# Optimization experiments

Hardware: AMD Instinct MI355X
Metric: run time of the kernel (lower is better)

## Reference

```python
import jax, jax.numpy as jnp
import numpy as np

N_NODES = 50000
N_EDGES = 400000
FEAT = 64      # irreps_in modeled as 64 scalar channels; head_dim == FEAT
HEADS = 4


def setup_inputs() -> dict:
    key = jax.random.key(0)
    k = jax.random.split(key, 7)
    x = jax.random.normal(k[0], (N_NODES, FEAT), dtype=jnp.float32)
    edge_index = jax.random.randint(k[1], (2, N_EDGES), 0, N_NODES, dtype=jnp.int32)
    s = 1.0 / np.sqrt(FEAT)
    Wq = jax.random.normal(k[2], (HEADS, FEAT, FEAT), dtype=jnp.float32) * s
    Wk = jax.random.normal(k[3], (HEADS, FEAT, FEAT), dtype=jnp.float32) * s
    Wv = jax.random.normal(k[4], (HEADS, FEAT, FEAT), dtype=jnp.float32) * s
    Wout = jax.random.normal(k[5], (FEAT, FEAT), dtype=jnp.float32) * s
    return {"x": x, "Wq": Wq, "Wk": Wk, "Wv": Wv, "Wout": Wout, "edge_index": edge_index}


def reference(x, Wq, Wk, Wv, Wout, edge_index):
    # Per-node attention over graph neighbors. The torch module pads neighbors
    # into degree buckets and runs SDPA per bucket; mathematically this is a
    # segment (per-receiver) softmax over incoming edges, which we compute
    # directly without padding or bucket loops.
    sender, receiver = edge_index[0], edge_index[1]
    n = x.shape[0]
    scale = x.shape[1] ** -0.5  # head_dim == FEAT in the original module

    Q = jnp.einsum('nf,hfd->hnd', x, Wq)  # (H, N, F)
    K = jnp.einsum('nf,hfd->hnd', x, Wk)
    V = jnp.einsum('nf,hfd->hnd', x, Wv)

    # Edge scores: q_receiver . k_sender per head -> (E, H)
    s = jnp.einsum('hef,hef->eh', Q[:, receiver], K[:, sender]) * scale

    # Numerically stable segment softmax over each receiver's neighborhood.
    m = jax.ops.segment_max(s, receiver, num_segments=n)          # (N, H)
    p = jnp.exp(s - m[receiver])                                   # (E, H)
    denom = jax.ops.segment_sum(p, receiver, num_segments=n)      # (N, H)
    alpha = p / denom[receiver]                                    # (E, H)

    # Weighted message aggregation: (H, E, F) scattered to (H, N, F).
    msg = alpha.T[:, :, None] * V[:, sender]
    agg = jax.vmap(lambda mh: jax.ops.segment_sum(mh, receiver, num_segments=n))(msg)

    out = jnp.nan_to_num(agg.mean(axis=0))  # deg-0 nodes contribute zeros
    return x + out @ Wout
```

## Files before the change

### kernel.cpp

```cpp
#include <hip/hip_runtime.h>

#define FEAT 64
#define HEADS 4
#define CAP 64
#define LROW 520
#define TSTR 80

typedef __attribute__((ext_vector_type(8))) short short8;
typedef __attribute__((ext_vector_type(8))) __bf16 bf16x8;
typedef __attribute__((ext_vector_type(4))) float floatx4;
typedef __attribute__((ext_vector_type(2))) float float2v;
typedef unsigned short ushortT;

static __device__ __forceinline__ unsigned short f2bf(float f) {
    union { float f; unsigned int u; } v; v.f = f;
    unsigned int u = v.u;
    u = u + 0x7fffu + ((u >> 16) & 1u);
    return (unsigned short)(u >> 16);
}
static __device__ __forceinline__ float bfl(unsigned int u) {
    union { unsigned int u; float f; } v; v.u = u << 16; return v.f;
}
static __device__ __forceinline__ float bfh(unsigned int u) {
    union { unsigned int u; float f; } v; v.u = u & 0xffff0000u; return v.f;
}

template <int CTRL>
static __device__ __forceinline__ float dppadd(float v) {
    int y = __builtin_amdgcn_update_dpp(0, __builtin_bit_cast(int, v),
                                        CTRL, 0xf, 0xf, true);
    return v + __builtin_bit_cast(float, y);
}

__global__ __launch_bounds__(256) void k_init(const float* __restrict__ Wq,
        const float* __restrict__ Wk, const float* __restrict__ Wv,
        const float* __restrict__ Wout, short8* __restrict__ Wpack,
        short8* __restrict__ WoutPack, int4* __restrict__ deg4, int nslots) {
    int t = blockIdx.x * 256 + threadIdx.x;
    if (t < nslots) deg4[t] = make_int4(0, 0, 0, 0);
    int o = t;
    if (o < 12 * 2 * 4 * 64) {
        int lane = o & 63, dt = (o >> 6) & 3, kb = (o >> 8) & 1, m = o >> 9;
        int mat = m >> 2, h = m & 3;
        const float* src = (mat == 0) ? Wq : (mat == 1) ? Wk : Wv;
        src += (size_t)h * 64 * 64;
        int d = dt * 16 + (lane & 15);
        int kbase = kb * 32 + (lane >> 4) * 8;
        short8 val;
#pragma unroll
        for (int j = 0; j < 8; j++)
            val[j] = (short)f2bf(src[(kbase + j) * 64 + d]);
        Wpack[o] = val;
    } else if (o < 6144 + 512) {
        int idx = o - 6144;
        int lane = idx & 63, kb = (idx >> 6) & 1, nt = idx >> 7;
        int d = nt * 16 + (lane & 15);
        int kbase = kb * 32 + (lane >> 4) * 8;
        short8 val;
#pragma unroll
        for (int j = 0; j < 8; j++)
            val[j] = (short)f2bf(Wout[(kbase + j) * 64 + d]);
        WoutPack[idx] = val;
    }
}

__global__ __launch_bounds__(256, 3) void k_qkv(const float* __restrict__ x,
        const short8* __restrict__ Wpack, const int* __restrict__ send,
        const int* __restrict__ recv, int* __restrict__ deg,
        int* __restrict__ srt, ushortT* __restrict__ Qb, ushortT* __restrict__ KVb,
        int E) {
    __shared__ ushortT lds[16 * LROW];
    int w = threadIdx.x >> 6, lane = threadIdx.x & 63;
    int quad = lane >> 4, lrow = lane & 15;
    int ntile = blockIdx.x * 16;

    int e = blockIdx.x * 256 + threadIdx.x;
    int r_edge = 0, s_edge = 0, pos = CAP;
    if (e < E) {
        r_edge = recv[e];
        s_edge = send[e];
        pos = atomicAdd(&deg[r_edge], 1);
    }

    const float* xrow = x + (size_t)(ntile + lrow) * 64 + quad * 8;
    float4 fa = *(const float4*)(xrow);
    float4 fb = *(const float4*)(xrow + 4);
    float4 fc = *(const float4*)(xrow + 32);
    float4 fd = *(const float4*)(xrow + 36);

    short8 B[3][2][4];
#pragma unroll
    for (int mat = 0; mat < 3; mat++)
#pragma unroll
        for (int kb = 0; kb < 2; kb++)
#pragma unroll
            for (int dt = 0; dt < 4; dt++)
                B[mat][kb][dt] =
                    Wpack[(((mat * 4 + w) * 2 + kb) * 4 + dt) * 64 + lane];

    short8 a0 = {(short)f2bf(fa.x), (short)f2bf(fa.y), (short)f2bf(fa.z), (short)f2bf(fa.w),
                 (short)f2bf(fb.x), (short)f2bf(fb.y), (short)f2bf(fb.z), (short)f2bf(fb.w)};
    short8 a1 = {(short)f2bf(fc.x), (short)f2bf(fc.y), (short)f2bf(fc.z), (short)f2bf(fc.w),
                 (short)f2bf(fd.x), (short)f2bf(fd.y), (short)f2bf(fd.z), (short)f2bf(fd.w)};
    bf16x8 X0 = __builtin_bit_cast(bf16x8, a0);
    bf16x8 X1 = __builtin_bit_cast(bf16x8, a1);
#pragma unroll
    for (int mat = 0; mat < 3; mat++) {
#pragma unroll
        for (int dt = 0; dt < 4; dt++) {
            floatx4 acc = {0.f, 0.f, 0.f, 0.f};
            acc = __builtin_amdgcn_mfma_f32_16x16x32_bf16(
                __builtin_bit_cast(bf16x8, B[mat][0][dt]), X0, acc, 0, 0, 0);
            acc = __builtin_amdgcn_mfma_f32_16x16x32_bf16(
                __builtin_bit_cast(bf16x8, B[mat][1][dt]), X1, acc, 0, 0, 0);
            if (mat == 0) {
                unsigned int u01 = (unsigned)f2bf(acc[0] * 0.125f)
                                 | ((unsigned)f2bf(acc[1] * 0.125f) << 16);
                unsigned int u23 = (unsigned)f2bf(acc[2] * 0.125f)
                                 | ((unsigned)f2bf(acc[3] * 0.125f) << 16);
                *(uint2*)&lds[lrow * LROW + w * 64 + dt * 16 + quad * 4]
                    = make_uint2(u01, u23);
            } else {
                int p = __builtin_amdgcn_cvt_pk_fp8_f32(acc[0], acc[1], 0, false);
                p = __builtin_amdgcn_cvt_pk_fp8_f32(acc[2], acc[3], p, true);
                int slot = w * 16 + dt * 4 + quad;
                *(unsigned int*)&lds[lrow * LROW + 256 + slot * 4 + ((mat == 2) ? 2 : 0)]
                    = (unsigned int)p;
            }
        }
    }
    __syncthreads();
    {
        int u = threadIdx.x;
#pragma unroll
        for (int rep = 0; rep < 2; rep++, u += 256) {
            int row = u >> 5, idx = u & 31;
            uint4 val = *(const uint4*)&lds[row * LROW + idx * 8];
            *(uint4*)(Qb + ((size_t)(ntile + row)) * 256 + idx * 8) = val;
        }
    }
    {
        uint4* KVq = (uint4*)KVb;
        int u = threadIdx.x;
#pragma unroll
        for (int rep = 0; rep < 2; rep++, u += 256) {
            int row = u >> 5, idx = u & 31;
            uint4 val = *(const uint4*)&lds[row * LROW + 256 + idx * 8];
            KVq[(size_t)(ntile + row) * 32 + idx] = val;
        }
    }
    if (e < E && pos < CAP) srt[(size_t)r_edge * CAP + pos] = s_edge;
}

__global__ __launch_bounds__(256, 3) void k_attn(const ushortT* __restrict__ Qb,
        const ushortT* __restrict__ KVb, const short8* __restrict__ WoutPack,
        const int* __restrict__ deg, const int* __restrict__ srt,
        const float* __restrict__ x, float* __restrict__ out, int N) {
    __shared__ ushortT tl[16 * TSTR];
    int w = threadIdx.x >> 6, lane = threadIdx.x & 63;
    int hs = lane >> 5, hl = lane & 31, jj = hl & 7;
    int rb = blockIdx.x * 16;
    const uint4* KV4 = (const uint4*)KVb;

    int d_[2]; uint4 qu_[2]; int4 sf_[2], s2_[2]; const int* slots_[2];
#pragma unroll
    for (int p = 0; p < 2; p++) {
        int r = rb + w * 4 + p * 2 + hs;
        d_[p] = min(deg[r], CAP);
        slots_[p] = srt + (size_t)r * CAP;
        qu_[p] = ((const uint4*)(Qb + (size_t)r * 256))[hl];
        sf_[p] = *(const int4*)(slots_[p]);
        s2_[p] = *(const int4*)(slots_[p] + 4);
    }

    uint4 kv_[2][8];
#pragma unroll
    for (int p = 0; p < 2; p++) {
        int d = d_[p];
        int s0 = (0 < d) ? sf_[p].x : 0;
        int s1 = (1 < d) ? sf_[p].y : 0;
        int s2v = (2 < d) ? sf_[p].z : 0;
        int s3 = (3 < d) ? sf_[p].w : 0;
        int s4v = (4 < d) ? s2_[p].x : 0;
        int s5 = (5 < d) ? s2_[p].y : 0;
        int s6 = (6 < d) ? s2_[p].z : 0;
        int s7 = (7 < d) ? s2_[p].w : 0;
        kv_[p][0] = KV4[(size_t)s0 * 32 + hl];
        kv_[p][1] = KV4[(size_t)s1 * 32 + hl];
        kv_[p][2] = KV4[(size_t)s2v * 32 + hl];
        kv_[p][3] = KV4[(size_t)s3 * 32 + hl];
        kv_[p][4] = KV4[(size_t)s4v * 32 + hl];
        kv_[p][5] = KV4[(size_t)s5 * 32 + hl];
        kv_[p][6] = KV4[(size_t)s6 * 32 + hl];
        kv_[p][7] = KV4[(size_t)s7 * 32 + hl];
    }

#pragma unroll
    for (int p = 0; p < 2; p++) {
        int d = d_[p];
        uint4 qu = qu_[p];
        float2v q01 = {bfl(qu.x), bfh(qu.x)};
        float2v q23 = {bfl(qu.y), bfh(qu.y)};
        float2v q45 = {bfl(qu.z), bfh(qu.z)};
        float2v q67 = {bfl(qu.w), bfh(qu.w)};
        float2v acc01 = {0.f, 0.f}, acc23 = {0.f, 0.f};
        float2v acc45 = {0.f, 0.f}, acc67 = {0.f, 0.f};
        float den = 0.f;

#define PROC(kv, pmask)                                                   \
    {                                                                     \
        float2v kA = __builtin_amdgcn_cvt_pk_f32_fp8(kv.x, false);        \
        float2v kB = __builtin_amdgcn_cvt_pk_f32_fp8(kv.x, true);         \
        float2v kC = __builtin_amdgcn_cvt_pk_f32_fp8(kv.z, false);        \
        float2v kD = __builtin_amdgcn_cvt_pk_f32_fp8(kv.z, true);         \
        float2v d2 = q01 * kA;                                            \
        d2 += q23 * kB;                                                   \
        d2 += q45 * kC;                                                   \
        d2 += q67 * kD;                                                   \
        float sp = d2.x + d2.y;                                           \
        sp = dppadd<0xB1>(sp);                                            \
        sp = dppadd<0x4E>(sp);                                            \
        sp = dppadd<0x141>(sp);                                           \
        float pv = __expf(sp);                                            \
        pv = (pmask) ? pv : 0.f;                                          \
        float2v vA = __builtin_amdgcn_cvt_pk_f32_fp8(kv.y, false);        \
        float2v vB = __builtin_amdgcn_cvt_pk_f32_fp8(kv.y, true);         \
        float2v vC = __builtin_amdgcn_cvt_pk_f32_fp8(kv.w, false);        \
        float2v vD = __builtin_amdgcn_cvt_pk_f32_fp8(kv.w, true);         \
        float2v pp = {pv, pv};                                            \
        den += pv;                                                        \
        acc01 += pp * vA; acc23 += pp * vB;                               \
        acc45 += pp * vC; acc67 += pp * vD;                               \
    }
        PROC(kv_[p][0], 0 < d) PROC(kv_[p][1], 1 < d)
        PROC(kv_[p][2], 2 < d) PROC(kv_[p][3], 3 < d)
        PROC(kv_[p][4], 4 < d) PROC(kv_[p][5], 5 < d)
        PROC(kv_[p][6], 6 < d) PROC(kv_[p][7], 7 < d)

        for (int i = 8; i < d; i += 4) {
            int4 s4 = *(const int4*)(slots_[p] + i);
            int t0 = s4.x;
            int t1 = (i + 1 < d) ? s4.y : 0;
            int t2 = (i + 2 < d) ? s4.z : 0;
            int t3 = (i + 3 < d) ? s4.w : 0;
            uint4 ka = KV4[(size_t)t0 * 32 + hl];
            uint4 kb = KV4[(size_t)t1 * 32 + hl];
            uint4 kc = KV4[(size_t)t2 * 32 + hl];
            uint4 kd = KV4[(size_t)t3 * 32 + hl];
            PROC(ka, true) PROC(kb, i + 1 < d) PROC(kc, i + 2 < d) PROC(kd, i + 3 < d)
        }
#undef PROC
        float a0 = acc01.x, a1 = acc01.y, a2 = acc23.x, a3 = acc23.y;
        float a4 = acc45.x, a5 = acc45.y, a6 = acc67.x, a7 = acc67.y;
        float inv = (den > 0.f) ? 0.25f / den : 0.f;
        a0 *= inv; a1 *= inv; a2 *= inv; a3 *= inv;
        a4 *= inv; a5 *= inv; a6 *= inv; a7 *= inv;
        a0 = dppadd<0x128>(a0); a1 = dppadd<0x128>(a1);
        a2 = dppadd<0x128>(a2); a3 = dppadd<0x128>(a3);
        a4 = dppadd<0x128>(a4); a5 = dppadd<0x128>(a5);
        a6 = dppadd<0x128>(a6); a7 = dppadd<0x128>(a7);
        a0 += __shfl_xor(a0, 16); a1 += __shfl_xor(a1, 16);
        a2 += __shfl_xor(a2, 16); a3 += __shfl_xor(a3, 16);
        a4 += __shfl_xor(a4, 16); a5 += __shfl_xor(a5, 16);
        a6 += __shfl_xor(a6, 16); a7 += __shfl_xor(a7, 16);
        if (hl < 8) {
            int ridx = w * 4 + p * 2 + hs;
            uint4 tv;
            tv.x = (unsigned)f2bf(a0) | ((unsigned)f2bf(a1) << 16);
            tv.y = (unsigned)f2bf(a2) | ((unsigned)f2bf(a3) << 16);
            tv.z = (unsigned)f2bf(a4) | ((unsigned)f2bf(a5) << 16);
            tv.w = (unsigned)f2bf(a6) | ((unsigned)f2bf(a7) << 16);
            *(uint4*)&tl[ridx * TSTR + jj * 8] = tv;
        }
    }
    __syncthreads();

    int q = lane >> 4, c = lane & 15;
    short8 ta0 = *(const short8*)&tl[c * TSTR + q * 8];
    short8 ta1 = *(const short8*)&tl[c * TSTR + 32 + q * 8];
    short8 tb0 = WoutPack[(w * 2 + 0) * 64 + lane];
    short8 tb1 = WoutPack[(w * 2 + 1) * 64 + lane];
    floatx4 acc = {0.f, 0.f, 0.f, 0.f};
    acc = __builtin_amdgcn_mfma_f32_16x16x32_bf16(
        __builtin_bit_cast(bf16x8, ta0), __builtin_bit_cast(bf16x8, tb0), acc, 0, 0, 0);
    acc = __builtin_amdgcn_mfma_f32_16x16x32_bf16(
        __builtin_bit_cast(bf16x8, ta1), __builtin_bit_cast(bf16x8, tb1), acc, 0, 0, 0);
#pragma unroll
    for (int reg = 0; reg < 4; reg++) {
        size_t idx = (size_t)(rb + q * 4 + reg) * 64 + w * 16 + c;
        out[idx] = x[idx] + acc[reg];
    }
}

extern "C" void kernel_launch(void* const* d_in, const int* in_sizes, int n_in,
                              void* d_out, int out_size, void* d_ws, size_t ws_size,
                              hipStream_t stream) {
    const float* x    = (const float*)d_in[0];
    const float* Wq   = (const float*)d_in[1];
    const float* Wk   = (const float*)d_in[2];
    const float* Wv   = (const float*)d_in[3];
    const float* Wout = (const float*)d_in[4];
    const int*   ei   = (const int*)d_in[5];
    int N = in_sizes[0] / FEAT;
    int E = in_sizes[5] / 2;
    const int* send = ei;
    const int* recv = ei + E;

    char* ws = (char*)d_ws;
    size_t o = 0;
    auto alloc = [&](size_t bytes) {
        void* p = ws + o;
        o = (o + bytes + 255) & ~(size_t)255;
        return p;
    };
    ushortT* Qb      = (ushortT*)alloc((size_t)N * 256 * 2);
    ushortT* KVb     = (ushortT*)alloc((size_t)N * 512);
    short8* Wpack    = (short8*)alloc(6144 * sizeof(short8));
    short8* WoutPack = (short8*)alloc(512 * sizeof(short8));
    int* deg         = (int*)alloc((size_t)((N + 3) & ~3) * 4);
    int* srt         = (int*)alloc((size_t)N * CAP * 4);

    int nslots = ((N + 3) & ~3) / 4;
    k_init<<<64, 256, 0, stream>>>(Wq, Wk, Wv, Wout, Wpack, WoutPack,
                                   (int4*)deg, nslots);
    k_qkv<<<N / 16, 256, 0, stream>>>(x, Wpack, send, recv, deg, srt, Qb, KVb, E);
    k_attn<<<N / 16, 256, 0, stream>>>(Qb, KVb, WoutPack, deg, srt, x,
                                       (float*)d_out, N);
}
```

Baseline: 142.3 us.

## Split edge scatter from projection kernel and decouple neighbor gathers from degree

The fused QKV-plus-edge-scatter kernel becomes two kernels: a dedicated edge scatter that builds per-receiver slot lists, and a pure projection kernel that loads weight fragments just before each MFMA instead of preloading all of them into registers. In the attention kernel, the first eight K/V gathers no longer wait on the degree load: slot indices are clamped to the valid node range instead of being masked by degree, so the gathers can issue as soon as the slot lists arrive. This relies on the later per-degree masking to discard the garbage slots. It also relaxes the attention kernel's occupancy hint and projection launch bounds, at the cost of an extra kernel launch and some wasted gather bandwidth on low-degree nodes.

```diff
diff --git a/kernel.cpp b/kernel.cpp
--- a/kernel.cpp
+++ b/kernel.cpp
@@ -64,40 +64,29 @@
     }
 }
 
-__global__ __launch_bounds__(256, 3) void k_qkv(const float* __restrict__ x,
-        const short8* __restrict__ Wpack, const int* __restrict__ send,
+__global__ __launch_bounds__(256) void k_scatter(const int* __restrict__ send,
         const int* __restrict__ recv, int* __restrict__ deg,
-        int* __restrict__ srt, ushortT* __restrict__ Qb, ushortT* __restrict__ KVb,
-        int E) {
+        int* __restrict__ srt, int E) {
+    int e = blockIdx.x * 256 + threadIdx.x;
+    if (e >= E) return;
+    int r = recv[e];
+    int s = send[e];
+    int pos = atomicAdd(&deg[r], 1);
+    if (pos < CAP) srt[(size_t)r * CAP + pos] = s;
+}
+
+__global__ __launch_bounds__(256) void k_proj(const float* __restrict__ x,
+        const short8* __restrict__ Wpack, ushortT* __restrict__ Qb,
+        ushortT* __restrict__ KVb) {
     __shared__ ushortT lds[16 * LROW];
     int w = threadIdx.x >> 6, lane = threadIdx.x & 63;
     int quad = lane >> 4, lrow = lane & 15;
     int ntile = blockIdx.x * 16;
-
-    int e = blockIdx.x * 256 + threadIdx.x;
-    int r_edge = 0, s_edge = 0, pos = CAP;
-    if (e < E) {
-        r_edge = recv[e];
-        s_edge = send[e];
-        pos = atomicAdd(&deg[r_edge], 1);
-    }
-
     const float* xrow = x + (size_t)(ntile + lrow) * 64 + quad * 8;
     float4 fa = *(const float4*)(xrow);
     float4 fb = *(const float4*)(xrow + 4);
     float4 fc = *(const float4*)(xrow + 32);
     float4 fd = *(const float4*)(xrow + 36);
-
-    short8 B[3][2][4];
-#pragma unroll
-    for (int mat = 0; mat < 3; mat++)
-#pragma unroll
-        for (int kb = 0; kb < 2; kb++)
-#pragma unroll
-            for (int dt = 0; dt < 4; dt++)
-                B[mat][kb][dt] =
-                    Wpack[(((mat * 4 + w) * 2 + kb) * 4 + dt) * 64 + lane];
-
     short8 a0 = {(short)f2bf(fa.x), (short)f2bf(fa.y), (short)f2bf(fa.z), (short)f2bf(fa.w),
                  (short)f2bf(fb.x), (short)f2bf(fb.y), (short)f2bf(fb.z), (short)f2bf(fb.w)};
     short8 a1 = {(short)f2bf(fc.x), (short)f2bf(fc.y), (short)f2bf(fc.z), (short)f2bf(fc.w),
@@ -106,13 +95,16 @@
     bf16x8 X1 = __builtin_bit_cast(bf16x8, a1);
 #pragma unroll
     for (int mat = 0; mat < 3; mat++) {
+        int m = mat * 4 + w;
 #pragma unroll
         for (int dt = 0; dt < 4; dt++) {
             floatx4 acc = {0.f, 0.f, 0.f, 0.f};
+            short8 b0 = Wpack[((m * 2 + 0) * 4 + dt) * 64 + lane];
+            short8 b1 = Wpack[((m * 2 + 1) * 4 + dt) * 64 + lane];
             acc = __builtin_amdgcn_mfma_f32_16x16x32_bf16(
-                __builtin_bit_cast(bf16x8, B[mat][0][dt]), X0, acc, 0, 0, 0);
+                __builtin_bit_cast(bf16x8, b0), X0, acc, 0, 0, 0);
             acc = __builtin_amdgcn_mfma_f32_16x16x32_bf16(
-                __builtin_bit_cast(bf16x8, B[mat][1][dt]), X1, acc, 0, 0, 0);
+                __builtin_bit_cast(bf16x8, b1), X1, acc, 0, 0, 0);
             if (mat == 0) {
                 unsigned int u01 = (unsigned)f2bf(acc[0] * 0.125f)
                                  | ((unsigned)f2bf(acc[1] * 0.125f) << 16);
@@ -149,10 +141,9 @@
             KVq[(size_t)(ntile + row) * 32 + idx] = val;
         }
     }
-    if (e < E && pos < CAP) srt[(size_t)r_edge * CAP + pos] = s_edge;
-}
-
-__global__ __launch_bounds__(256, 3) void k_attn(const ushortT* __restrict__ Qb,
+}
+
+__global__ __launch_bounds__(256, 2) void k_attn(const ushortT* __restrict__ Qb,
         const ushortT* __restrict__ KVb, const short8* __restrict__ WoutPack,
         const int* __restrict__ deg, const int* __restrict__ srt,
         const float* __restrict__ x, float* __restrict__ out, int N) {
@@ -166,25 +157,24 @@
 #pragma unroll
     for (int p = 0; p < 2; p++) {
         int r = rb + w * 4 + p * 2 + hs;
-        d_[p] = min(deg[r], CAP);
         slots_[p] = srt + (size_t)r * CAP;
-        qu_[p] = ((const uint4*)(Qb + (size_t)r * 256))[hl];
         sf_[p] = *(const int4*)(slots_[p]);
         s2_[p] = *(const int4*)(slots_[p] + 4);
+        qu_[p] = ((const uint4*)(Qb + (size_t)r * 256))[hl];
+        d_[p] = min(deg[r], CAP);
     }
 
     uint4 kv_[2][8];
 #pragma unroll
     for (int p = 0; p < 2; p++) {
-        int d = d_[p];
-        int s0 = (0 < d) ? sf_[p].x : 0;
-        int s1 = (1 < d) ? sf_[p].y : 0;
-        int s2v = (2 < d) ? sf_[p].z : 0;
-        int s3 = (3 < d) ? sf_[p].w : 0;
-        int s4v = (4 < d) ? s2_[p].x : 0;
-        int s5 = (5 < d) ? s2_[p].y : 0;
-        int s6 = (6 < d) ? s2_[p].z : 0;
-        int s7 = (7 < d) ? s2_[p].w : 0;
+        int s0 = min(max(sf_[p].x, 0), N - 1);
+        int s1 = min(max(sf_[p].y, 0), N - 1);
+        int s2v = min(max(sf_[p].z, 0), N - 1);
+        int s3 = min(max(sf_[p].w, 0), N - 1);
+        int s4v = min(max(s2_[p].x, 0), N - 1);
+        int s5 = min(max(s2_[p].y, 0), N - 1);
+        int s6 = min(max(s2_[p].z, 0), N - 1);
+        int s7 = min(max(s2_[p].w, 0), N - 1);
         kv_[p][0] = KV4[(size_t)s0 * 32 + hl];
         kv_[p][1] = KV4[(size_t)s1 * 32 + hl];
         kv_[p][2] = KV4[(size_t)s2v * 32 + hl];
@@ -323,7 +313,8 @@
     int nslots = ((N + 3) & ~3) / 4;
     k_init<<<64, 256, 0, stream>>>(Wq, Wk, Wv, Wout, Wpack, WoutPack,
                                    (int4*)deg, nslots);
-    k_qkv<<<N / 16, 256, 0, stream>>>(x, Wpack, send, recv, deg, srt, Qb, KVb, E);
+    k_scatter<<<(E + 255) / 256, 256, 0, stream>>>(send, recv, deg, srt, E);
+    k_proj<<<N / 16, 256, 0, stream>>>(x, Wpack, Qb, KVb);
     k_attn<<<N / 16, 256, 0, stream>>>(Qb, KVb, WoutPack, deg, srt, x,
                                        (float*)d_out, N);
 }
```

Result: slower. 152.0 us (+6.8%).

## Compute Q projection inside attention kernel instead of materializing it globally

Applied to the files above, without the earlier changes.

The Q projection moves from the projection kernel into the attention kernel. Each block computes Q for its own 16 receiver rows with MFMA into shared memory, so the bf16 Q buffer is no longer written to and read back from global memory. Q is computed while the KV gathers are in flight, which may hide some of that latency, but it adds a __syncthreads and extra MFMA work to the attention kernel. The launch bounds also drop the min-blocks hint of 3 and weights are loaded per tile instead of held up front, which changes register pressure and occupancy.

```diff
diff --git a/kernel.cpp b/kernel.cpp
--- a/kernel.cpp
+++ b/kernel.cpp
@@ -3,7 +3,8 @@
 #define FEAT 64
 #define HEADS 4
 #define CAP 64
-#define LROW 520
+#define KROW 264
+#define QROW 264
 #define TSTR 80
 
 typedef __attribute__((ext_vector_type(8))) short short8;
@@ -64,12 +65,11 @@
     }
 }
 
-__global__ __launch_bounds__(256, 3) void k_qkv(const float* __restrict__ x,
+__global__ __launch_bounds__(256) void k_proj(const float* __restrict__ x,
         const short8* __restrict__ Wpack, const int* __restrict__ send,
         const int* __restrict__ recv, int* __restrict__ deg,
-        int* __restrict__ srt, ushortT* __restrict__ Qb, ushortT* __restrict__ KVb,
-        int E) {
-    __shared__ ushortT lds[16 * LROW];
+        int* __restrict__ srt, ushortT* __restrict__ KVb, int E) {
+    __shared__ ushortT lds[16 * KROW];
     int w = threadIdx.x >> 6, lane = threadIdx.x & 63;
     int quad = lane >> 4, lrow = lane & 15;
     int ntile = blockIdx.x * 16;
@@ -87,17 +87,6 @@
     float4 fb = *(const float4*)(xrow + 4);
     float4 fc = *(const float4*)(xrow + 32);
     float4 fd = *(const float4*)(xrow + 36);
-
-    short8 B[3][2][4];
-#pragma unroll
-    for (int mat = 0; mat < 3; mat++)
-#pragma unroll
-        for (int kb = 0; kb < 2; kb++)
-#pragma unroll
-            for (int dt = 0; dt < 4; dt++)
-                B[mat][kb][dt] =
-                    Wpack[(((mat * 4 + w) * 2 + kb) * 4 + dt) * 64 + lane];
-
     short8 a0 = {(short)f2bf(fa.x), (short)f2bf(fa.y), (short)f2bf(fa.z), (short)f2bf(fa.w),
                  (short)f2bf(fb.x), (short)f2bf(fb.y), (short)f2bf(fb.z), (short)f2bf(fb.w)};
     short8 a1 = {(short)f2bf(fc.x), (short)f2bf(fc.y), (short)f2bf(fc.z), (short)f2bf(fc.w),
@@ -105,72 +94,58 @@
     bf16x8 X0 = __builtin_bit_cast(bf16x8, a0);
     bf16x8 X1 = __builtin_bit_cast(bf16x8, a1);
 #pragma unroll
-    for (int mat = 0; mat < 3; mat++) {
+    for (int mat = 1; mat < 3; mat++) {
+        int m = mat * 4 + w;
 #pragma unroll
         for (int dt = 0; dt < 4; dt++) {
             floatx4 acc = {0.f, 0.f, 0.f, 0.f};
+            short8 b0 = Wpack[((m * 2 + 0) * 4 + dt) * 64 + lane];
+            short8 b1 = Wpack[((m * 2 + 1) * 4 + dt) * 64 + lane];
             acc = __builtin_amdgcn_mfma_f32_16x16x32_bf16(
-                __builtin_bit_cast(bf16x8, B[mat][0][dt]), X0, acc, 0, 0, 0);
+                __builtin_bit_cast(bf16x8, b0), X0, acc, 0, 0, 0);
             acc = __builtin_amdgcn_mfma_f32_16x16x32_bf16(
-                __builtin_bit_cast(bf16x8, B[mat][1][dt]), X1, acc, 0, 0, 0);
-            if (mat == 0) {
-                unsigned int u01 = (unsigned)f2bf(acc[0] * 0.125f)
-                                 | ((unsigned)f2bf(acc[1] * 0.125f) << 16);
-                unsigned int u23 = (unsigned)f2bf(acc[2] * 0.125f)
-                                 | ((unsigned)f2bf(acc[3] * 0.125f) << 16);
-                *(uint2*)&lds[lrow * LROW + w * 64 + dt * 16 + quad * 4]
-                    = make_uint2(u01, u23);
-            } else {
-                int p = __builtin_amdgcn_cvt_pk_fp8_f32(acc[0], acc[1], 0, false);
-                p = __builtin_amdgcn_cvt_pk_fp8_f32(acc[2], acc[3], p, true);
-                int slot = w * 16 + dt * 4 + quad;
-                *(unsigned int*)&lds[lrow * LROW + 256 + slot * 4 + ((mat == 2) ? 2 : 0)]
-                    = (unsigned int)p;
-            }
+                __builtin_bit_cast(bf16x8, b1), X1, acc, 0, 0, 0);
+            int p = __builtin_amdgcn_cvt_pk_fp8_f32(acc[0], acc[1], 0, false);
+            p = __builtin_amdgcn_cvt_pk_fp8_f32(acc[2], acc[3], p, true);
+            int slot = w * 16 + dt * 4 + quad;
+            *(unsigned int*)&lds[lrow * KROW + slot * 4 + ((mat == 2) ? 2 : 0)]
+                = (unsigned int)p;
         }
     }
     __syncthreads();
-    {
-        int u = threadIdx.x;
-#pragma unroll
-        for (int rep = 0; rep < 2; rep++, u += 256) {
-            int row = u >> 5, idx = u & 31;
-            uint4 val = *(const uint4*)&lds[row * LROW + idx * 8];
-            *(uint4*)(Qb + ((size_t)(ntile + row)) * 256 + idx * 8) = val;
-        }
-    }
     {
         uint4* KVq = (uint4*)KVb;
         int u = threadIdx.x;
 #pragma unroll
         for (int rep = 0; rep < 2; rep++, u += 256) {
             int row = u >> 5, idx = u & 31;
-            uint4 val = *(const uint4*)&lds[row * LROW + 256 + idx * 8];
+            uint4 val = *(const uint4*)&lds[row * KROW + idx * 8];
             KVq[(size_t)(ntile + row) * 32 + idx] = val;
         }
     }
     if (e < E && pos < CAP) srt[(size_t)r_edge * CAP + pos] = s_edge;
 }
 
-__global__ __launch_bounds__(256, 3) void k_attn(const ushortT* __restrict__ Qb,
-        const ushortT* __restrict__ KVb, const short8* __restrict__ WoutPack,
+__global__ __launch_bounds__(256) void k_attn(const ushortT* __restrict__ KVb,
+        const short8* __restrict__ Wpack, const short8* __restrict__ WoutPack,
         const int* __restrict__ deg, const int* __restrict__ srt,
         const float* __restrict__ x, float* __restrict__ out, int N) {
+    __shared__ ushortT qt[16 * QROW];
     __shared__ ushortT tl[16 * TSTR];
     int w = threadIdx.x >> 6, lane = threadIdx.x & 63;
+    int quad = lane >> 4, lrow = lane & 15;
     int hs = lane >> 5, hl = lane & 31, jj = hl & 7;
     int rb = blockIdx.x * 16;
     const uint4* KV4 = (const uint4*)KVb;
 
-    int d_[2]; uint4 qu_[2]; int4 sf_[2], s2_[2]; const int* slots_[2];
+    int d_[2]; int4 sf_[2], s2_[2]; const int* slots_[2];
 #pragma unroll
     for (int p = 0; p < 2; p++) {
         int r = rb + w * 4 + p * 2 + hs;
-        d_[p] = min(deg[r], CAP);
         slots_[p] = srt + (size_t)r * CAP;
-        qu_[p] = ((const uint4*)(Qb + (size_t)r * 256))[hl];
         sf_[p] = *(const int4*)(slots_[p]);
         s2_[p] = *(const int4*)(slots_[p] + 4);
+        d_[p] = min(deg[r], CAP);
     }
 
     uint4 kv_[2][8];
@@ -193,6 +168,47 @@
         kv_[p][5] = KV4[(size_t)s5 * 32 + hl];
         kv_[p][6] = KV4[(size_t)s6 * 32 + hl];
         kv_[p][7] = KV4[(size_t)s7 * 32 + hl];
+    }
+
+    {
+        const float* xrow = x + (size_t)(rb + lrow) * 64 + quad * 8;
+        float4 fa = *(const float4*)(xrow);
+        float4 fb = *(const float4*)(xrow + 4);
+        float4 fc = *(const float4*)(xrow + 32);
+        float4 fd = *(const float4*)(xrow + 36);
+        short8 bq0[4], bq1[4];
+#pragma unroll
+        for (int dt = 0; dt < 4; dt++) {
+            bq0[dt] = Wpack[((w * 2 + 0) * 4 + dt) * 64 + lane];
+            bq1[dt] = Wpack[((w * 2 + 1) * 4 + dt) * 64 + lane];
+        }
+        short8 a0 = {(short)f2bf(fa.x), (short)f2bf(fa.y), (short)f2bf(fa.z), (short)f2bf(fa.w),
+                     (short)f2bf(fb.x), (short)f2bf(fb.y), (short)f2bf(fb.z), (short)f2bf(fb.w)};
+        short8 a1 = {(short)f2bf(fc.x), (short)f2bf(fc.y), (short)f2bf(fc.z), (short)f2bf(fc.w),
+                     (short)f2bf(fd.x), (short)f2bf(fd.y), (short)f2bf(fd.z), (short)f2bf(fd.w)};
+        bf16x8 X0 = __builtin_bit_cast(bf16x8, a0);
+        bf16x8 X1 = __builtin_bit_cast(bf16x8, a1);
+#pragma unroll
+        for (int dt = 0; dt < 4; dt++) {
+            floatx4 acc = {0.f, 0.f, 0.f, 0.f};
+            acc = __builtin_amdgcn_mfma_f32_16x16x32_bf16(
+                __builtin_bit_cast(bf16x8, bq0[dt]), X0, acc, 0, 0, 0);
+            acc = __builtin_amdgcn_mfma_f32_16x16x32_bf16(
+                __builtin_bit_cast(bf16x8, bq1[dt]), X1, acc, 0, 0, 0);
+            unsigned int u01 = (unsigned)f2bf(acc[0] * 0.125f)
+                             | ((unsigned)f2bf(acc[1] * 0.125f) << 16);
+            unsigned int u23 = (unsigned)f2bf(acc[2] * 0.125f)
+                             | ((unsigned)f2bf(acc[3] * 0.125f) << 16);
+            *(uint2*)&qt[lrow * QROW + w * 64 + dt * 16 + quad * 4]
+                = make_uint2(u01, u23);
+        }
+    }
+    __syncthreads();
+    uint4 qu_[2];
+#pragma unroll
+    for (int p = 0; p < 2; p++) {
+        int ridx = w * 4 + p * 2 + hs;
+        qu_[p] = *(const uint4*)&qt[ridx * QROW + hl * 8];
     }
 
 #pragma unroll
@@ -313,7 +329,6 @@
         o = (o + bytes + 255) & ~(size_t)255;
         return p;
     };
-    ushortT* Qb      = (ushortT*)alloc((size_t)N * 256 * 2);
     ushortT* KVb     = (ushortT*)alloc((size_t)N * 512);
     short8* Wpack    = (short8*)alloc(6144 * sizeof(short8));
     short8* WoutPack = (short8*)alloc(512 * sizeof(short8));
@@ -323,7 +338,7 @@
     int nslots = ((N + 3) & ~3) / 4;
     k_init<<<64, 256, 0, stream>>>(Wq, Wk, Wv, Wout, Wpack, WoutPack,
                                    (int4*)deg, nslots);
-    k_qkv<<<N / 16, 256, 0, stream>>>(x, Wpack, send, recv, deg, srt, Qb, KVb, E);
-    k_attn<<<N / 16, 256, 0, stream>>>(Qb, KVb, WoutPack, deg, srt, x,
+    k_proj<<<N / 16, 256, 0, stream>>>(x, Wpack, send, recv, deg, srt, KVb, E);
+    k_attn<<<N / 16, 256, 0, stream>>>(KVb, Wpack, WoutPack, deg, srt, x,
                                        (float*)d_out, N);
 }
```

After: 141.5 us. No clear change (-0.6%).
